# Optimization experiments

Hardware: AMD Instinct MI355X
Metric: run time of the kernel (lower is better)

Reference implementation:

```python
import jax, jax.numpy as jnp
import numpy as np

B, S, H = 4, 1024, 1024
NHEADS = 16
DK = H // NHEADS


def setup_inputs() -> dict:
    key = jax.random.key(0)
    ks = jax.random.split(key, 9)
    scale = 1.0 / np.sqrt(H).astype(np.float32)
    query = jax.random.normal(ks[0], (B, S, H), dtype=jnp.float32)
    key_in = jax.random.normal(ks[1], (B, S, H), dtype=jnp.float32)
    score_mask = jax.random.randint(ks[2], (B, S, S), 0, 2).astype(bool)
    # torch nn.Linear params, stored as [in, out] so y = x @ W + b
    Wq = jax.random.normal(ks[3], (H, H), dtype=jnp.float32) * scale
    bq = jax.random.normal(ks[4], (H,), dtype=jnp.float32) * scale
    Wk = jax.random.normal(ks[5], (H, H), dtype=jnp.float32) * scale
    bk = jax.random.normal(ks[6], (H,), dtype=jnp.float32) * scale
    Wp = jax.random.normal(ks[7], (H, H), dtype=jnp.float32) * scale
    bp = jax.random.normal(ks[8], (H,), dtype=jnp.float32) * scale
    return dict(query=query, key_in=key_in, score_mask=score_mask,
                Wq=Wq, bq=bq, Wk=Wk, bk=bk, Wp=Wp, bp=bp)


def reference(query, key_in, score_mask, Wq, bq, Wk, bk, Wp, bp):
    # Projections + head split: [B,S,H] -> [B,h,S,dk]
    q = (query @ Wq + bq).reshape(B, S, NHEADS, DK).transpose(0, 2, 1, 3)
    k = (key_in @ Wk + bk).reshape(B, S, NHEADS, DK).transpose(0, 2, 1, 3)
    inv_sqrt_dk = jnp.asarray(1.0 / np.sqrt(DK), dtype=q.dtype)
    scores = jnp.einsum('bhqd,bhkd->bhqk', q, k) * inv_sqrt_dk
    # masked_fill(score_mask.unsqueeze(1), -1e9): mask True = masked, broadcast over heads
    scores = jnp.where(score_mask[:, None, :, :], jnp.asarray(-1e9, scores.dtype), scores)
    # redundant per-row mask multiply: b = ~mask[:, None, :, 0:1]
    row_keep = (~score_mask[:, None, :, 0:1]).astype(scores.dtype)  # [B,1,S,1]
    p_attn = jax.nn.softmax(scores, axis=-1) * row_keep
    # NON-STANDARD: value is the projected query, not a separate value tensor
    out = jnp.einsum('bhqk,bhkd->bhqd', p_attn, q)
    out = out.transpose(0, 2, 1, 3).reshape(B, S, H)  # merge heads
    return out @ Wp + bp
```

## Files before the change

kernel.cpp:

```cpp
#include <hip/hip_runtime.h>
#include <hip/hip_bf16.h>

using bf16x8 = __attribute__((ext_vector_type(8))) short;
using f32x4  = __attribute__((ext_vector_type(4))) float;

static __device__ __forceinline__ short f2bf(float f) {
  union { float f; unsigned u; } x; x.f = f;
  unsigned r = x.u + 0x7fffu + ((x.u >> 16) & 1u);
  return (short)(r >> 16);
}
static __device__ __forceinline__ float bf2f(short b) {
  union { unsigned u; float f; } x; x.u = ((unsigned)(unsigned short)b) << 16;
  return x.f;
}
static __device__ __forceinline__ unsigned pack_bf2(float lo, float hi) {
  __hip_bfloat162 h = __float22bfloat162_rn(float2{lo, hi});
  unsigned u; __builtin_memcpy(&u, &h, 4); return u;
}
static __device__ __forceinline__ float exp2_raw(float x) {
  float r; asm("v_exp_f32 %0, %1" : "=v"(r) : "v"(x)); return r;
}
static __device__ __forceinline__ void gll16(const void* g, void* l) {
  __builtin_amdgcn_global_load_lds((__attribute__((address_space(1))) const void*)g,
                                   (__attribute__((address_space(3))) void*)l, 16, 0, 0);
}

__global__ void k_prep(const float* __restrict__ query, const float* __restrict__ key_in,
                       const float* __restrict__ Wq, const float* __restrict__ Wk,
                       const float* __restrict__ Wp,
                       const unsigned* __restrict__ mask_u32,
                       short* __restrict__ Qbf, short* __restrict__ Kbf,
                       short* __restrict__ Wt3, unsigned long long* __restrict__ packb) {
  const int bid = blockIdx.x, tid = threadIdx.x;
  if (bid < 2048) {
    const float* in = bid < 1024 ? query : key_in;
    short* out = bid < 1024 ? Qbf : Kbf;
    const int r = bid & 1023;
    const int n4 = (4 * 1024 * 1024) / 4;
    for (int i = r * 256 + tid; i < n4; i += 1024 * 256) {
      float4 v = reinterpret_cast<const float4*>(in)[i];
      short4 o;
      o.x = f2bf(v.x); o.y = f2bf(v.y); o.z = f2bf(v.z); o.w = f2bf(v.w);
      reinterpret_cast<short4*>(out)[i] = o;
    }
  } else if (bid < 5120) {
    __shared__ float tile[32][33];
    const int sub = bid - 2048;
    const int w = sub >> 10, s2 = sub & 1023;
    const int bx = s2 & 31, by = s2 >> 5;
    const float* in = w == 0 ? Wq : (w == 1 ? Wk : Wp);
    short* out = Wt3 + (size_t)w * 1024 * 1024;
    const int tx = tid & 31, ty = tid >> 5;
    int x = bx * 32 + tx, y0 = by * 32;
    for (int j = 0; j < 32; j += 8)
      tile[ty + j][tx] = in[(size_t)(y0 + ty + j) * 1024 + x];
    __syncthreads();
    int xo = by * 32 + tx, yo = bx * 32;
    for (int j = 0; j < 32; j += 8)
      out[(size_t)(yo + ty + j) * 1024 + xo] = f2bf(tile[tx][ty + j]);
  } else {
    const int r = bid - 5120;
    unsigned probe = mask_u32[tid & 63];
    const bool u8mode = (__ballot(probe > 1u) != 0ull);
    const unsigned char* s8 = (const unsigned char*)mask_u32;
    const int* s32 = (const int*)mask_u32;
    const int n = 4 * 1024 * 1024;
    for (int e = r * 256 + tid; e < n; e += 2048 * 256) {
      int v = u8mode ? (int)s8[e] : s32[e];
      unsigned long long b = __ballot(v != 0);
      if ((tid & 63) == 0) packb[e >> 6] = b;
    }
  }
}

template<int OUT_BF16, int BN, int M, int N, int K, int VT_OUT>
__device__ __forceinline__ void gemm_body(const short* __restrict__ A,
                                          const short* __restrict__ Bt,
                                          const float* __restrict__ bias,
                                          void* __restrict__ C,
                                          short* __restrict__ Vtg,
                                          short* __restrict__ Al,
                                          short* __restrict__ Bl) {
  constexpr int JF = BN / 32;
  const int tid  = threadIdx.x;
  const int lane = tid & 63, wid = tid >> 6;
  const int g = lane >> 4, lr = lane & 15;
  const int wm = wid >> 1, wn = wid & 1;
  constexpr int nbx = N / BN;
  constexpr int nwg = nbx * (M >> 7);
  const int lin = blockIdx.y * nbx + blockIdx.x;
  const int orig = (lin & 7) * (nwg >> 3) + (lin >> 3);
  const int m0 = (orig / nbx) * 128, n0 = (orig % nbx) * BN;
  const int srow = lane >> 3;
  const int sch  = ((lane & 7) ^ srow) * 8;

  f32x4 acc[4][JF];
#pragma unroll
  for (int i = 0; i < 4; ++i)
#pragma unroll
    for (int j = 0; j < JF; ++j) acc[i][j] = (f32x4){0.f, 0.f, 0.f, 0.f};

  constexpr int NT = K >> 6;
  auto stage = [&](int buf, int kt) {
#pragma unroll
    for (int s = 0; s < 4; ++s)
      gll16(&A[(size_t)(m0 + s * 32 + wid * 8 + srow) * K + kt + sch],
            &Al[buf * 128 * 64 + (s * 32 + wid * 8) * 64]);
#pragma unroll
    for (int s = 0; s < BN / 32; ++s)
      gll16(&Bt[(size_t)(n0 + s * 32 + wid * 8 + srow) * K + kt + sch],
            &Bl[buf * BN * 64 + (s * 32 + wid * 8) * 64]);
  };

  stage(0, 0);
  asm volatile("s_waitcnt vmcnt(0)" ::: "memory");
  __builtin_amdgcn_s_barrier();
  asm volatile("" ::: "memory");

#pragma unroll 1
  for (int t = 0; t < NT; ++t) {
    const int cur = t & 1;
    if (t + 1 < NT) stage(cur ^ 1, (t + 1) * 64);
#pragma unroll
    for (int kb = 0; kb < 2; ++kb) {
      const int cs = ((kb * 4 + g) ^ (lr & 7)) * 8;
      bf16x8 af[4], bfr[JF];
#pragma unroll
      for (int i = 0; i < 4; ++i)
        af[i] = *reinterpret_cast<const bf16x8*>(
            &Al[cur * 128 * 64 + (wm * 64 + i * 16 + lr) * 64 + cs]);
#pragma unroll
      for (int j = 0; j < JF; ++j)
        bfr[j] = *reinterpret_cast<const bf16x8*>(
            &Bl[cur * BN * 64 + (wn * (BN / 2) + j * 16 + lr) * 64 + cs]);
#pragma unroll
      for (int i = 0; i < 4; ++i)
#pragma unroll
        for (int j = 0; j < JF; ++j)
          acc[i][j] = __builtin_amdgcn_mfma_f32_16x16x32_bf16(af[i], bfr[j], acc[i][j], 0, 0, 0);
    }
    if (t + 1 < NT) {
      asm volatile("s_waitcnt vmcnt(0)" ::: "memory");
      __builtin_amdgcn_s_barrier();
      asm volatile("" ::: "memory");
    }
  }

#pragma unroll
  for (int i = 0; i < 4; ++i) {
    int row = m0 + wm * 64 + i * 16 + g * 4;
#pragma unroll
    for (int j = 0; j < JF; ++j) {
      int col = n0 + wn * (BN / 2) + j * 16 + lr;
      float bv = bias[col];
#pragma unroll
      for (int r = 0; r < 4; ++r) {
        float v = acc[i][j][r] + bv;
        if (OUT_BF16) ((short*)C)[(size_t)(row + r) * N + col] = f2bf(v);
        else          ((float*)C)[(size_t)(row + r) * N + col] = v;
      }
    }
  }

  if (VT_OUT) {
    short* T = Al;
    __builtin_amdgcn_s_barrier();
    asm volatile("" ::: "memory");
#pragma unroll
    for (int i = 0; i < 4; ++i) {
      int row = wm * 64 + i * 16 + g * 4;
#pragma unroll
      for (int j = 0; j < JF; ++j) {
        int col = wn * (BN / 2) + j * 16 + lr;
        float bv = bias[n0 + col];
        unsigned d0 = pack_bf2(acc[i][j][0] + bv, acc[i][j][1] + bv);
        unsigned d1 = pack_bf2(acc[i][j][2] + bv, acc[i][j][3] + bv);
        unsigned long long w = (unsigned long long)d0 | ((unsigned long long)d1 << 32);
        *reinterpret_cast<unsigned long long*>(
            &T[col * 128 + (row ^ ((col & 7) << 4))]) = w;
      }
    }
    __builtin_amdgcn_s_barrier();
    asm volatile("" ::: "memory");
    const int bb = m0 >> 10, s0 = m0 & 1023, h0 = n0 >> 6;
#pragma unroll
    for (int it = 0; it < 8; ++it) {
      int ch = it * 256 + tid;
      int d_loc = ch >> 4, sc = ch & 15;
      bf16x8 v = *reinterpret_cast<const bf16x8*>(
          &T[d_loc * 128 + ((sc * 8) ^ ((d_loc & 7) << 4))]);
      *reinterpret_cast<bf16x8*>(
          &Vtg[(size_t)((bb * 16 + h0 + (d_loc >> 6)) * 64 + (d_loc & 63)) * 1024
               + s0 + sc * 8]) = v;
    }
  }
}

__launch_bounds__(256)
__global__ void k_gemm_qk(const short* __restrict__ A0, const short* __restrict__ A1,
                          const short* __restrict__ Bt3,
                          const float* __restrict__ b0, const float* __restrict__ b1,
                          short* __restrict__ C0, short* __restrict__ C1,
                          short* __restrict__ Vtg) {
  __shared__ short Al[2][128 * 64];
  __shared__ short Bl[2][128 * 64];
  if (blockIdx.z == 0)
    gemm_body<1, 128, 4096, 1024, 1024, 1>(A0, Bt3, b0, C0, Vtg,
                                           &Al[0][0], &Bl[0][0]);
  else
    gemm_body<1, 128, 4096, 1024, 1024, 0>(A1, Bt3 + 1024 * 1024, b1, C1, nullptr,
                                           &Al[0][0], &Bl[0][0]);
}

__launch_bounds__(256)
__global__ void k_gemm_out(const short* __restrict__ A, const short* __restrict__ Bt,
                           const float* __restrict__ bias, float* __restrict__ C) {
  __shared__ short Al[2][128 * 64];
  __shared__ short Bl[2][64 * 64];
  gemm_body<0, 64, 4096, 1024, 1024, 0>(A, Bt, bias, C, nullptr,
                                        &Al[0][0], &Bl[0][0]);
}

__launch_bounds__(512)
__global__ void k_attention(const short* __restrict__ Qp, const short* __restrict__ Kp,
                            const short* __restrict__ Vtg,
                            const unsigned long long* __restrict__ mb,
                            short* __restrict__ O) {
  __shared__ short Kl[2][2][64 * 64];
  __shared__ short Vl[2][2][64 * 64];
  __shared__ short Pl[8][16 * 64];
  const int tid  = threadIdx.x;
  const int lane = tid & 63, wid = tid >> 6;
  const int g = lane >> 4, lr = lane & 15;
  const int g4 = 4 * g;
  const int bid = (blockIdx.x & 7) * 64 + (blockIdx.x >> 3);
  const int qt = bid & 7, h = (bid >> 3) & 15, b = bid >> 7;
  const int qb = qt * 128 + wid * 16;
  const int srow = lane >> 3;
  const int sch  = ((lane & 7) ^ srow) * 8;

  const size_t qrow = (size_t)(b * 1024 + qb + lr);
  const float qs = 0.125f * 1.44269504088896340736f;
  bf16x8 aq[2];
#pragma unroll
  for (int db = 0; db < 2; ++db) {
    bf16x8 raw = *reinterpret_cast<const bf16x8*>(&Qp[qrow * 1024 + h * 64 + db * 32 + g * 8]);
#pragma unroll
    for (int j = 0; j < 8; j += 2) {
      unsigned pk = pack_bf2(bf2f(raw[j]) * qs, bf2f(raw[j + 1]) * qs);
      aq[db][j]     = (short)(pk & 0xffffu);
      aq[db][j + 1] = (short)(pk >> 16);
    }
  }

  const unsigned long long* mrow = &mb[qrow * 16];
  const short* Ksrc = &Kp[(size_t)(b * 1024 + wid * 8 + srow) * 1024 + h * 64 + sch];
  const short* Vsrc = &Vtg[(size_t)((b * 16 + h) * 64 + wid * 8 + srow) * 1024 + sch];

  f32x4 o[4];
#pragma unroll
  for (int d = 0; d < 4; ++d) o[d] = (f32x4){0.f, 0.f, 0.f, 0.f};
  float l_part = 0.f;
  short* Prow = &Pl[wid][lr * 64];

  gll16(Ksrc,                           &Kl[0][0][(wid * 8) * 64]);
  gll16(Ksrc + (size_t)64 * 1024,       &Kl[0][1][(wid * 8) * 64]);
  gll16(Vsrc,                           &Vl[0][0][(wid * 8) * 64]);
  gll16(Vsrc + 64,                      &Vl[0][1][(wid * 8) * 64]);
  unsigned long long mwA0 = mrow[0], mwA1 = mrow[1];
  unsigned long long mwB0 = 0, mwB1 = 0;
  const float keep = (mwA0 & 1ull) ? 0.f : 1.f;

#pragma unroll 1
  for (int kt = 0; kt < 8; ++kt) {
    const int cur = kt & 1;
    if (kt < 7) asm volatile("s_waitcnt vmcnt(2)" ::: "memory");
    else        asm volatile("s_waitcnt vmcnt(0)" ::: "memory");
    __builtin_amdgcn_s_barrier();
    asm volatile("" ::: "memory");

    if (kt + 1 < 8) {
      const size_t kb128 = (size_t)(kt + 1) * 128;
      gll16(Ksrc + kb128 * 1024,              &Kl[cur ^ 1][0][(wid * 8) * 64]);
      gll16(Ksrc + (kb128 + 64) * 1024,       &Kl[cur ^ 1][1][(wid * 8) * 64]);
      gll16(Vsrc + kb128,                     &Vl[cur ^ 1][0][(wid * 8) * 64]);
      gll16(Vsrc + kb128 + 64,                &Vl[cur ^ 1][1][(wid * 8) * 64]);
      mwB0 = mrow[2 * kt + 2];
      mwB1 = mrow[2 * kt + 3];
    }

#pragma unroll
    for (int hk = 0; hk < 2; ++hk) {
      const unsigned long long mwfull = hk ? mwA1 : mwA0;
      const unsigned mlo = (unsigned)mwfull;
      const unsigned mhi = (unsigned)(mwfull >> 32);
      const short* Kb = Kl[cur][hk];
      const short* Vb = Vl[cur][hk];

#pragma unroll
      for (int kc = 0; kc < 4; ++kc) {
        f32x4 a = (f32x4){0.f, 0.f, 0.f, 0.f};
        __builtin_amdgcn_s_setprio(1);
#pragma unroll
        for (int db = 0; db < 2; ++db) {
          bf16x8 kf = *reinterpret_cast<const bf16x8*>(
              &Kb[(kc * 16 + lr) * 64 + (((db * 4 + g) ^ (lr & 7)) * 8)]);
          a = __builtin_amdgcn_mfma_f32_16x16x32_bf16(kf, aq[db], a, 0, 0, 0);
        }
        __builtin_amdgcn_s_setprio(0);
        const unsigned wk = ((kc < 2 ? mlo : mhi) >> (((kc & 1) << 4) + g4)) & 0xFu;
        float p0 = (wk & 1u) ? 0.f : exp2_raw(a[0]);
        float p1 = (wk & 2u) ? 0.f : exp2_raw(a[1]);
        float p2 = (wk & 4u) ? 0.f : exp2_raw(a[2]);
        float p3 = (wk & 8u) ? 0.f : exp2_raw(a[3]);
        l_part += (p0 + p1) + (p2 + p3);
        unsigned lo = pack_bf2(p0, p1), hi = pack_bf2(p2, p3);
        unsigned long long w = (unsigned long long)lo | ((unsigned long long)hi << 32);
        *reinterpret_cast<unsigned long long*>(
            &Prow[((2 * kc + (g >> 1)) ^ (lr & 7)) * 8 + (g & 1) * 4]) = w;
      }

      __builtin_amdgcn_s_setprio(1);
#pragma unroll
      for (int kb = 0; kb < 2; ++kb) {
        bf16x8 pa = *reinterpret_cast<const bf16x8*>(
            &Prow[(((kb * 4 + g) ^ (lr & 7)) * 8)]);
        const int cs = ((kb * 4 + g) ^ (lr & 7)) * 8;
#pragma unroll
        for (int d = 0; d < 4; ++d) {
          bf16x8 vf = *reinterpret_cast<const bf16x8*>(&Vb[(d * 16 + lr) * 64 + cs]);
          o[d] = __builtin_amdgcn_mfma_f32_16x16x32_bf16(vf, pa, o[d], 0, 0, 0);
        }
      }
      __builtin_amdgcn_s_setprio(0);
    }
    mwA0 = mwB0; mwA1 = mwB1;
    asm volatile("" ::: "memory");
  }

  float l_run = l_part;
  l_run += __shfl_xor(l_run, 16);
  l_run += __shfl_xor(l_run, 32);

  const float inv = (l_run > 0.f) ? keep / l_run : 0.f;
#pragma unroll
  for (int d = 0; d < 4; ++d) {
    unsigned lo = pack_bf2(o[d][0] * inv, o[d][1] * inv);
    unsigned hi = pack_bf2(o[d][2] * inv, o[d][3] * inv);
    unsigned long long w = (unsigned long long)lo | ((unsigned long long)hi << 32);
    *reinterpret_cast<unsigned long long*>(
        &Prow[((2 * d + (g >> 1)) ^ (lr & 7)) * 8 + (g & 1) * 4]) = w;
  }
#pragma unroll
  for (int it = 0; it < 2; ++it) {
    int qq = it * 8 + srow;
    bf16x8 val = *reinterpret_cast<const bf16x8*>(
        &Pl[wid][qq * 64 + (((lane & 7) ^ (qq & 7)) * 8)]);
    *reinterpret_cast<bf16x8*>(
        &O[(size_t)(b * 1024 + qt * 128 + wid * 16 + qq) * 1024 + h * 64 + (lane & 7) * 8]) = val;
  }
}

extern "C" void kernel_launch(void* const* d_in, const int* in_sizes, int n_in,
                              void* d_out, int out_size, void* d_ws, size_t ws_size,
                              hipStream_t stream) {
  const float* query  = (const float*)d_in[0];
  const float* key_in = (const float*)d_in[1];
  const void*  mask_raw = d_in[2];
  const float* Wq = (const float*)d_in[3];
  const float* bq = (const float*)d_in[4];
  const float* Wk = (const float*)d_in[5];
  const float* bk = (const float*)d_in[6];
  const float* Wp = (const float*)d_in[7];
  const float* bp = (const float*)d_in[8];

  char* ws = (char*)d_ws;
  size_t off = 0;
  auto alloc = [&](size_t bytes) {
    char* p = ws + off;
    off = (off + bytes + 255) & ~(size_t)255;
    return p;
  };
  unsigned long long* packb = (unsigned long long*)alloc(512ull << 10);
  short* Qbf   = (short*)alloc(8ull << 20);
  short* Kbf   = (short*)alloc(8ull << 20);
  short* Wt3   = (short*)alloc(6ull << 20);
  short* Qproj = (short*)alloc(8ull << 20);
  short* Kproj = (short*)alloc(8ull << 20);
  short* Vtg   = (short*)alloc(8ull << 20);
  short* AttnO = Kbf;

  k_prep<<<7168, 256, 0, stream>>>(query, key_in, Wq, Wk, Wp,
                                   (const unsigned*)mask_raw, Qbf, Kbf, Wt3, packb);

  dim3 gqk(8, 32, 2);
  k_gemm_qk<<<gqk, 256, 0, stream>>>(Qbf, Kbf, Wt3, bq, bk, Qproj, Kproj, Vtg);

  k_attention<<<512, 512, 0, stream>>>(Qproj, Kproj, Vtg, packb, AttnO);

  k_gemm_out<<<dim3(16, 32), 256, 0, stream>>>(AttnO, Wt3 + 2 * 1024 * 1024, bp,
                                               (float*)d_out);
}
```

Before: 93.23 us.

## Switch attention to 32x32x16 MFMA with 4 waves of 32 query rows

Restructures the attention kernel so each of 4 waves handles 32 query rows using 32x32x16 bf16 MFMA for both QK^T and PV, instead of 8 waves of 16 rows using 16x16x32 MFMA. Block size drops from 512 to 256 threads, each thread issues more K/V loads per tile, and the wait is now vmcnt(0) before each barrier. The larger MFMA shape is meant to improve operand reuse and cut LDS fragment reads per flop, at the cost of more accumulator registers per wave and fewer waves per block to hide latency.

Result: slower. 98.97 us (+6.1%).

```diff
diff --git a/kernel.cpp b/kernel.cpp
--- a/kernel.cpp
+++ b/kernel.cpp
@@ -3,6 +3,7 @@
 
 using bf16x8 = __attribute__((ext_vector_type(8))) short;
 using f32x4  = __attribute__((ext_vector_type(4))) float;
+using f32x16 = __attribute__((ext_vector_type(16))) float;
 
 static __device__ __forceinline__ short f2bf(float f) {
   union { float f; unsigned u; } x; x.f = f;
@@ -221,52 +222,56 @@
                                         &Al[0][0], &Bl[0][0]);
 }
 
-__launch_bounds__(512)
+__launch_bounds__(256)
 __global__ void k_attention(const short* __restrict__ Qp, const short* __restrict__ Kp,
                             const short* __restrict__ Vtg,
                             const unsigned long long* __restrict__ mb,
                             short* __restrict__ O) {
-  __shared__ short Kl[2][2][64 * 64];
+  __shared__ short Kl[2][128 * 64];
   __shared__ short Vl[2][2][64 * 64];
-  __shared__ short Pl[8][16 * 64];
+  __shared__ short Pl[4][32 * 64];
   const int tid  = threadIdx.x;
   const int lane = tid & 63, wid = tid >> 6;
-  const int g = lane >> 4, lr = lane & 15;
-  const int g4 = 4 * g;
+  const int q31 = lane & 31, h2 = lane >> 5;
+  const int qsw = q31 & 7;
   const int bid = (blockIdx.x & 7) * 64 + (blockIdx.x >> 3);
   const int qt = bid & 7, h = (bid >> 3) & 15, b = bid >> 7;
-  const int qb = qt * 128 + wid * 16;
-  const int srow = lane >> 3;
-  const int sch  = ((lane & 7) ^ srow) * 8;
-
-  const size_t qrow = (size_t)(b * 1024 + qb + lr);
+  const int srow8 = tid >> 3;
+  const int sch   = ((tid & 7) ^ (srow8 & 7)) * 8;
+
+  const size_t qrow = (size_t)(b * 1024 + qt * 128 + wid * 32 + q31);
   const float qs = 0.125f * 1.44269504088896340736f;
-  bf16x8 aq[2];
-#pragma unroll
-  for (int db = 0; db < 2; ++db) {
-    bf16x8 raw = *reinterpret_cast<const bf16x8*>(&Qp[qrow * 1024 + h * 64 + db * 32 + g * 8]);
+  bf16x8 aq[4];
+#pragma unroll
+  for (int ks = 0; ks < 4; ++ks) {
+    bf16x8 raw = *reinterpret_cast<const bf16x8*>(
+        &Qp[qrow * 1024 + h * 64 + ks * 16 + h2 * 8]);
 #pragma unroll
     for (int j = 0; j < 8; j += 2) {
       unsigned pk = pack_bf2(bf2f(raw[j]) * qs, bf2f(raw[j + 1]) * qs);
-      aq[db][j]     = (short)(pk & 0xffffu);
-      aq[db][j + 1] = (short)(pk >> 16);
+      aq[ks][j]     = (short)(pk & 0xffffu);
+      aq[ks][j + 1] = (short)(pk >> 16);
     }
   }
 
   const unsigned long long* mrow = &mb[qrow * 16];
-  const short* Ksrc = &Kp[(size_t)(b * 1024 + wid * 8 + srow) * 1024 + h * 64 + sch];
-  const short* Vsrc = &Vtg[(size_t)((b * 16 + h) * 64 + wid * 8 + srow) * 1024 + sch];
-
-  f32x4 o[4];
-#pragma unroll
-  for (int d = 0; d < 4; ++d) o[d] = (f32x4){0.f, 0.f, 0.f, 0.f};
+  const short* Ksrc = &Kp[(size_t)(b * 1024 + srow8) * 1024 + h * 64 + sch];
+  const short* Vsrc = &Vtg[(size_t)((b * 16 + h) * 64 + srow8) * 1024 + sch];
+
+  f32x16 o0, o1;
+#pragma unroll
+  for (int j = 0; j < 16; ++j) { o0[j] = 0.f; o1[j] = 0.f; }
   float l_part = 0.f;
-  short* Prow = &Pl[wid][lr * 64];
-
-  gll16(Ksrc,                           &Kl[0][0][(wid * 8) * 64]);
-  gll16(Ksrc + (size_t)64 * 1024,       &Kl[0][1][(wid * 8) * 64]);
-  gll16(Vsrc,                           &Vl[0][0][(wid * 8) * 64]);
-  gll16(Vsrc + 64,                      &Vl[0][1][(wid * 8) * 64]);
+  short* Prow = &Pl[wid][0];
+
+  gll16(Ksrc,                         &Kl[0][(wid * 8) * 64]);
+  gll16(Ksrc + (size_t)32 * 1024,     &Kl[0][(32 + wid * 8) * 64]);
+  gll16(Ksrc + (size_t)64 * 1024,     &Kl[0][(64 + wid * 8) * 64]);
+  gll16(Ksrc + (size_t)96 * 1024,     &Kl[0][(96 + wid * 8) * 64]);
+  gll16(Vsrc,                         &Vl[0][0][(wid * 8) * 64]);
+  gll16(Vsrc + (size_t)32 * 1024,     &Vl[0][0][(32 + wid * 8) * 64]);
+  gll16(Vsrc + 64,                    &Vl[0][1][(wid * 8) * 64]);
+  gll16(Vsrc + (size_t)32 * 1024 + 64, &Vl[0][1][(32 + wid * 8) * 64]);
   unsigned long long mwA0 = mrow[0], mwA1 = mrow[1];
   unsigned long long mwB0 = 0, mwB1 = 0;
   const float keep = (mwA0 & 1ull) ? 0.f : 1.f;
@@ -274,90 +279,103 @@
 #pragma unroll 1
   for (int kt = 0; kt < 8; ++kt) {
     const int cur = kt & 1;
-    if (kt < 7) asm volatile("s_waitcnt vmcnt(2)" ::: "memory");
-    else        asm volatile("s_waitcnt vmcnt(0)" ::: "memory");
+    asm volatile("s_waitcnt vmcnt(0)" ::: "memory");
     __builtin_amdgcn_s_barrier();
     asm volatile("" ::: "memory");
 
     if (kt + 1 < 8) {
-      const size_t kb128 = (size_t)(kt + 1) * 128;
-      gll16(Ksrc + kb128 * 1024,              &Kl[cur ^ 1][0][(wid * 8) * 64]);
-      gll16(Ksrc + (kb128 + 64) * 1024,       &Kl[cur ^ 1][1][(wid * 8) * 64]);
-      gll16(Vsrc + kb128,                     &Vl[cur ^ 1][0][(wid * 8) * 64]);
-      gll16(Vsrc + kb128 + 64,                &Vl[cur ^ 1][1][(wid * 8) * 64]);
+      const short* Ks = Ksrc + (size_t)(kt + 1) * 128 * 1024;
+      const short* Vs = Vsrc + (kt + 1) * 128;
+      gll16(Ks,                          &Kl[cur ^ 1][(wid * 8) * 64]);
+      gll16(Ks + (size_t)32 * 1024,      &Kl[cur ^ 1][(32 + wid * 8) * 64]);
+      gll16(Ks + (size_t)64 * 1024,      &Kl[cur ^ 1][(64 + wid * 8) * 64]);
+      gll16(Ks + (size_t)96 * 1024,      &Kl[cur ^ 1][(96 + wid * 8) * 64]);
+      gll16(Vs,                          &Vl[cur ^ 1][0][(wid * 8) * 64]);
+      gll16(Vs + (size_t)32 * 1024,      &Vl[cur ^ 1][0][(32 + wid * 8) * 64]);
+      gll16(Vs + 64,                     &Vl[cur ^ 1][1][(wid * 8) * 64]);
+      gll16(Vs + (size_t)32 * 1024 + 64, &Vl[cur ^ 1][1][(32 + wid * 8) * 64]);
       mwB0 = mrow[2 * kt + 2];
       mwB1 = mrow[2 * kt + 3];
     }
 
 #pragma unroll
     for (int hk = 0; hk < 2; ++hk) {
-      const unsigned long long mwfull = hk ? mwA1 : mwA0;
-      const unsigned mlo = (unsigned)mwfull;
-      const unsigned mhi = (unsigned)(mwfull >> 32);
-      const short* Kb = Kl[cur][hk];
+      const unsigned long long mw = hk ? mwA1 : mwA0;
+      const short* Kb = &Kl[cur][hk * 64 * 64];
       const short* Vb = Vl[cur][hk];
 
 #pragma unroll
-      for (int kc = 0; kc < 4; ++kc) {
-        f32x4 a = (f32x4){0.f, 0.f, 0.f, 0.f};
+      for (int kb2 = 0; kb2 < 2; ++kb2) {
+        f32x16 s;
+#pragma unroll
+        for (int j = 0; j < 16; ++j) s[j] = 0.f;
         __builtin_amdgcn_s_setprio(1);
 #pragma unroll
-        for (int db = 0; db < 2; ++db) {
+        for (int ks = 0; ks < 4; ++ks) {
           bf16x8 kf = *reinterpret_cast<const bf16x8*>(
-              &Kb[(kc * 16 + lr) * 64 + (((db * 4 + g) ^ (lr & 7)) * 8)]);
-          a = __builtin_amdgcn_mfma_f32_16x16x32_bf16(kf, aq[db], a, 0, 0, 0);
+              &Kb[(kb2 * 32 + q31) * 64 + (((2 * ks + h2) ^ qsw) * 8)]);
+          s = __builtin_amdgcn_mfma_f32_32x32x16_bf16(kf, aq[ks], s, 0, 0, 0);
         }
         __builtin_amdgcn_s_setprio(0);
-        const unsigned wk = ((kc < 2 ? mlo : mhi) >> (((kc & 1) << 4) + g4)) & 0xFu;
-        float p0 = (wk & 1u) ? 0.f : exp2_raw(a[0]);
-        float p1 = (wk & 2u) ? 0.f : exp2_raw(a[1]);
-        float p2 = (wk & 4u) ? 0.f : exp2_raw(a[2]);
-        float p3 = (wk & 8u) ? 0.f : exp2_raw(a[3]);
-        l_part += (p0 + p1) + (p2 + p3);
-        unsigned lo = pack_bf2(p0, p1), hi = pack_bf2(p2, p3);
-        unsigned long long w = (unsigned long long)lo | ((unsigned long long)hi << 32);
-        *reinterpret_cast<unsigned long long*>(
-            &Prow[((2 * kc + (g >> 1)) ^ (lr & 7)) * 8 + (g & 1) * 4]) = w;
-      }
-
-      __builtin_amdgcn_s_setprio(1);
-#pragma unroll
-      for (int kb = 0; kb < 2; ++kb) {
-        bf16x8 pa = *reinterpret_cast<const bf16x8*>(
-            &Prow[(((kb * 4 + g) ^ (lr & 7)) * 8)]);
-        const int cs = ((kb * 4 + g) ^ (lr & 7)) * 8;
-#pragma unroll
-        for (int d = 0; d < 4; ++d) {
-          bf16x8 vf = *reinterpret_cast<const bf16x8*>(&Vb[(d * 16 + lr) * 64 + cs]);
-          o[d] = __builtin_amdgcn_mfma_f32_16x16x32_bf16(vf, pa, o[d], 0, 0, 0);
+        const unsigned long long mh = mw >> (kb2 * 32 + h2 * 4);
+#pragma unroll
+        for (int r2 = 0; r2 < 4; ++r2) {
+          const unsigned wk = (unsigned)(mh >> (8 * r2)) & 0xFu;
+          float p0 = (wk & 1u) ? 0.f : exp2_raw(s[4 * r2]);
+          float p1 = (wk & 2u) ? 0.f : exp2_raw(s[4 * r2 + 1]);
+          float p2 = (wk & 4u) ? 0.f : exp2_raw(s[4 * r2 + 2]);
+          float p3 = (wk & 8u) ? 0.f : exp2_raw(s[4 * r2 + 3]);
+          l_part += (p0 + p1) + (p2 + p3);
+          unsigned lo = pack_bf2(p0, p1), hi = pack_bf2(p2, p3);
+          unsigned long long w = (unsigned long long)lo | ((unsigned long long)hi << 32);
+          *reinterpret_cast<unsigned long long*>(
+              &Prow[q31 * 64 + (((4 * kb2 + r2) ^ qsw) * 8) + 4 * h2]) = w;
         }
       }
+
+      __builtin_amdgcn_s_setprio(1);
+#pragma unroll
+      for (int ks = 0; ks < 4; ++ks) {
+        bf16x8 pa = *reinterpret_cast<const bf16x8*>(
+            &Prow[q31 * 64 + (((2 * ks + h2) ^ qsw) * 8)]);
+        bf16x8 v0 = *reinterpret_cast<const bf16x8*>(
+            &Vb[q31 * 64 + (((2 * ks + h2) ^ qsw) * 8)]);
+        o0 = __builtin_amdgcn_mfma_f32_32x32x16_bf16(v0, pa, o0, 0, 0, 0);
+        bf16x8 v1 = *reinterpret_cast<const bf16x8*>(
+            &Vb[(32 + q31) * 64 + (((2 * ks + h2) ^ qsw) * 8)]);
+        o1 = __builtin_amdgcn_mfma_f32_32x32x16_bf16(v1, pa, o1, 0, 0, 0);
+      }
       __builtin_amdgcn_s_setprio(0);
     }
     mwA0 = mwB0; mwA1 = mwB1;
     asm volatile("" ::: "memory");
   }
 
-  float l_run = l_part;
-  l_run += __shfl_xor(l_run, 16);
-  l_run += __shfl_xor(l_run, 32);
-
+  float l_run = l_part + __shfl_xor(l_part, 32);
   const float inv = (l_run > 0.f) ? keep / l_run : 0.f;
-#pragma unroll
-  for (int d = 0; d < 4; ++d) {
-    unsigned lo = pack_bf2(o[d][0] * inv, o[d][1] * inv);
-    unsigned hi = pack_bf2(o[d][2] * inv, o[d][3] * inv);
-    unsigned long long w = (unsigned long long)lo | ((unsigned long long)hi << 32);
-    *reinterpret_cast<unsigned long long*>(
-        &Prow[((2 * d + (g >> 1)) ^ (lr & 7)) * 8 + (g & 1) * 4]) = w;
-  }
-#pragma unroll
-  for (int it = 0; it < 2; ++it) {
-    int qq = it * 8 + srow;
+
+#pragma unroll
+  for (int db = 0; db < 2; ++db) {
+#pragma unroll
+    for (int r2 = 0; r2 < 4; ++r2) {
+      float a0 = (db ? o1[4 * r2]     : o0[4 * r2])     * inv;
+      float a1 = (db ? o1[4 * r2 + 1] : o0[4 * r2 + 1]) * inv;
+      float a2 = (db ? o1[4 * r2 + 2] : o0[4 * r2 + 2]) * inv;
+      float a3 = (db ? o1[4 * r2 + 3] : o0[4 * r2 + 3]) * inv;
+      unsigned lo = pack_bf2(a0, a1), hi = pack_bf2(a2, a3);
+      unsigned long long w = (unsigned long long)lo | ((unsigned long long)hi << 32);
+      *reinterpret_cast<unsigned long long*>(
+          &Prow[q31 * 64 + (((4 * db + r2) ^ qsw) * 8) + 4 * h2]) = w;
+    }
+  }
+#pragma unroll
+  for (int it = 0; it < 4; ++it) {
+    int idx = it * 64 + lane;
+    int qq = idx >> 3, c = idx & 7;
     bf16x8 val = *reinterpret_cast<const bf16x8*>(
-        &Pl[wid][qq * 64 + (((lane & 7) ^ (qq & 7)) * 8)]);
+        &Prow[qq * 64 + ((c ^ (qq & 7)) * 8)]);
     *reinterpret_cast<bf16x8*>(
-        &O[(size_t)(b * 1024 + qt * 128 + wid * 16 + qq) * 1024 + h * 64 + (lane & 7) * 8]) = val;
+        &O[(size_t)(b * 1024 + qt * 128 + wid * 32 + qq) * 1024 + h * 64 + c * 8]) = val;
   }
 }
 
@@ -396,7 +414,7 @@
   dim3 gqk(8, 32, 2);
   k_gemm_qk<<<gqk, 256, 0, stream>>>(Qbf, Kbf, Wt3, bq, bk, Qproj, Kproj, Vtg);
 
-  k_attention<<<512, 512, 0, stream>>>(Qproj, Kproj, Vtg, packb, AttnO);
+  k_attention<<<512, 256, 0, stream>>>(Qproj, Kproj, Vtg, packb, AttnO);
 
   k_gemm_out<<<dim3(16, 32), 256, 0, stream>>>(AttnO, Wt3 + 2 * 1024 * 1024, bp,
                                                (float*)d_out);
```
